# Performance work log

Hardware: AMD Instinct MI355X
Metric: run time of the kernel (lower is better)

The kernel has to match this reference:

```python
import jax, jax.numpy as jnp
import numpy as np

NUM_HEADS = 16
FOCUS_FACTOR = 1.6
HEAD_REGION = {0: 0, 1: 1, 2: 2}  # head -> region (first/middle/end)


def setup_inputs() -> dict:
    key = jax.random.key(0)
    k1, k2, k3, k4, k5 = jax.random.split(key, 5)
    B, S, D = 2, 2048, 1024
    # GPT-2 style init scale so softmax is not fully saturated
    return {
        "hidden_states": jax.random.normal(k1, (B, S, D), dtype=jnp.float32),
        "c_attn_w": jax.random.normal(k2, (D, 3 * D), dtype=jnp.float32) * 0.02,
        "c_attn_b": jax.random.normal(k3, (3 * D,), dtype=jnp.float32) * 0.02,
        "c_proj_w": jax.random.normal(k4, (D, D), dtype=jnp.float32) * 0.02,
        "c_proj_b": jax.random.normal(k5, (D,), dtype=jnp.float32) * 0.02,
    }


def _region_multipliers(seq_len: int, num_heads: int, factor: float) -> jnp.ndarray:
    """[H, S] multiplier: selected heads up-weight their token region."""
    first_end = max(1, seq_len // 3)
    second_end = max(first_end + 1, 2 * seq_len // 3)
    pos = jnp.arange(seq_len)
    regions = [
        pos < first_end,
        (pos >= first_end) & (pos < second_end),
        pos >= second_end,
    ]
    mult = np.ones((num_heads, seq_len), dtype=np.float32)
    mult = jnp.asarray(mult)
    for h, r in HEAD_REGION.items():
        if h < num_heads:
            mult = mult.at[h].set(1.0 + (factor - 1.0) * regions[r].astype(jnp.float32))
    return mult


def reference(hidden_states, c_attn_w, c_attn_b, c_proj_w, c_proj_b):
    B, S, D = hidden_states.shape
    H = NUM_HEADS
    hd = D // H

    qkv = hidden_states @ c_attn_w + c_attn_b  # [B, S, 3D]
    q, k, v = jnp.split(qkv, 3, axis=-1)

    def _reshape(x):  # [B, S, D] -> [B, H, S, hd]
        return x.reshape(B, S, H, hd).transpose(0, 2, 1, 3)

    q, k, v = _reshape(q), _reshape(k), _reshape(v)

    scores = jnp.einsum("bhqd,bhkd->bhqk", q, k) / jnp.sqrt(jnp.float32(hd))
    causal = jnp.tril(jnp.ones((S, S), dtype=bool))
    mask_value = jnp.finfo(scores.dtype).min
    scores = jnp.where(causal[None, None], scores, mask_value)

    attn = jax.nn.softmax(scores, axis=-1)  # [B, H, S, S]

    # Per-head region reweight + renorm (only for the divergent heads)
    mult = _region_multipliers(S, H, FOCUS_FACTOR)  # [H, S]
    scaled = attn * mult[None, :, None, :]
    scaled = scaled / jnp.sum(scaled, axis=-1, keepdims=True)
    div_heads = jnp.zeros((H,), dtype=bool)
    for h in HEAD_REGION:
        if h < H:
            div_heads = div_heads.at[h].set(True)
    attn = jnp.where(div_heads[None, :, None, None], scaled, attn)

    out = jnp.einsum("bhqk,bhkd->bhqd", attn, v)  # [B, H, S, hd]
    out = out.transpose(0, 2, 1, 3).reshape(B, S, D)
    out = out @ c_proj_w + c_proj_b
    return out
```

## Files before the change

kernel.cpp:

```cpp
#include <hip/hip_runtime.h>
#include <hip/hip_bf16.h>

typedef __attribute__((ext_vector_type(8))) short bf16x8;
typedef __attribute__((ext_vector_type(4))) float f32x4;
typedef __attribute__((ext_vector_type(16))) float f32x16;
typedef __attribute__((ext_vector_type(4))) unsigned int u32x4;
typedef unsigned short u16;

#define MFMA_BF16(a, b, c) __builtin_amdgcn_mfma_f32_16x16x32_bf16(a, b, c, 0, 0, 0)
#define MFMA32(a, b, c) __builtin_amdgcn_mfma_f32_32x32x16_bf16(a, b, c, 0, 0, 0)

__device__ inline u16 f2b(float x) {
  unsigned int u = __builtin_bit_cast(unsigned int, x);
  u += 0x7fffu + ((u >> 16) & 1u);
  return (u16)(u >> 16);
}

__device__ inline float exp2_fast(float x) {
  float r;
  asm("v_exp_f32 %0, %1" : "=v"(r) : "v"(x));
  return r;
}

__device__ inline unsigned int cvtpk_bf16(float lo, float hi) {
  unsigned int r;
  asm("v_cvt_pk_bf16_f32 %0, %1, %2" : "=v"(r) : "v"(lo), "v"(hi));
  return r;
}

__device__ inline void pswap(unsigned int& dst, unsigned int& src) {
  asm("v_permlane32_swap_b32 %0, %1" : "+v"(dst), "+v"(src));
}

__device__ inline void gload16(void* lds, const void* g) {
  __builtin_amdgcn_global_load_lds((const __attribute__((address_space(1))) void*)g,
                                   (__attribute__((address_space(3))) void*)lds,
                                   16, 0, 0);
}


__global__ __launch_bounds__(256) void cast_f32_bf16(const float* __restrict__ src,
                                                     u16* __restrict__ dst, int n4) {
  int i = blockIdx.x * blockDim.x + threadIdx.x;
  if (i < n4) {
    float4 v = ((const float4*)src)[i];
    ushort4 o;
    o.x = f2b(v.x); o.y = f2b(v.y); o.z = f2b(v.z); o.w = f2b(v.w);
    ((ushort4*)dst)[i] = o;
  }
}

__global__ __launch_bounds__(256) void transpose_cast(const float* __restrict__ src,
                                                      u16* __restrict__ dst, int K, int N) {
  __shared__ float t[32][33];
  int k0 = blockIdx.x * 32, n0 = blockIdx.y * 32;
  int tx = threadIdx.x, ty = threadIdx.y;
#pragma unroll
  for (int i = 0; i < 4; i++) t[ty + i * 8][tx] = src[(size_t)(k0 + ty + i * 8) * N + n0 + tx];
  __syncthreads();
#pragma unroll
  for (int i = 0; i < 4; i++)
    dst[(size_t)(n0 + ty + i * 8) * K + k0 + tx] = f2b(t[tx][ty + i * 8]);
}

#define QSCALE 0.1803368801f

__global__ __launch_bounds__(512, 2) void gemm256_qkv(
    const u16* __restrict__ A, const u16* __restrict__ BT, const float* __restrict__ bias,
    u16* __restrict__ oQ, u16* __restrict__ oK, u16* __restrict__ oVf) {
  __shared__ __align__(16) u16 As[2][256 * 64];
  __shared__ __align__(16) u16 Bs[2][256 * 64];
  const int K = 1024, NT = 16;
  int tid = threadIdx.x;
  int wv = tid >> 6, lane = tid & 63, lr = lane & 15, lg = lane >> 4;
  int wm = wv >> 2, wn = wv & 3;
  int bx = blockIdx.x % 12, by = blockIdx.x / 12;
  int m0 = by * 256, n0 = bx * 256;

  f32x4 acc[8][4] = {};

  auto stageA = [&](int buf, int kt, int h) {
#pragma unroll
    for (int g = 0; g < 2; g++) {
      int li = g * 512 + tid;
      int row = (li >> 3) + h * 128;
      int cb = ((li & 7) * 16) ^ ((row & 7) << 4);
      gload16((char*)&As[buf][0] + h * 16384 + g * 8192 + wv * 1024,
              (const char*)(A + (size_t)(m0 + row) * K + kt * 64) + cb);
    }
  };
  auto stageB = [&](int buf, int kt, int h) {
#pragma unroll
    for (int g = 0; g < 2; g++) {
      int li = g * 512 + tid;
      int row = (li >> 3) + h * 128;
      int cb = ((li & 7) * 16) ^ ((row & 7) << 4);
      gload16((char*)&Bs[buf][0] + h * 16384 + g * 8192 + wv * 1024,
              (const char*)(BT + (size_t)(n0 + row) * K + kt * 64) + cb);
    }
  };

  stageA(0, 0, 0); stageB(0, 0, 0); stageB(0, 0, 1); stageA(0, 0, 1);

  for (int t = 0; t < NT; ++t) {
    const int buf = t & 1;
    const bool last = (t == NT - 1);
    const char* Ab = (const char*)&As[buf][0];
    const char* Bb = (const char*)&Bs[buf][0];
    bf16x8 a[4][2], b0[2][2], b1[2][2];

    if (last) asm volatile("s_waitcnt vmcnt(0)" ::: "memory");
    else      asm volatile("s_waitcnt vmcnt(4)" ::: "memory");
    __builtin_amdgcn_s_barrier();
#pragma unroll
    for (int ii = 0; ii < 4; ii++) {
      int row = wm * 16 + ii * 32 + lr;
#pragma unroll
      for (int kk = 0; kk < 2; kk++)
        a[ii][kk] = *(const bf16x8*)(Ab + row * 128 + ((kk * 64 + lg * 16) ^ ((row & 7) << 4)));
    }
#pragma unroll
    for (int jj2 = 0; jj2 < 2; jj2++) {
      int row = wn * 16 + jj2 * 64 + lr;
#pragma unroll
      for (int kk = 0; kk < 2; kk++)
        b0[jj2][kk] = *(const bf16x8*)(Bb + row * 128 + ((kk * 64 + lg * 16) ^ ((row & 7) << 4)));
    }
    if (!last) stageA(buf ^ 1, t + 1, 0);
    __builtin_amdgcn_s_setprio(1);
#pragma unroll
    for (int ii = 0; ii < 4; ii++)
#pragma unroll
      for (int jj2 = 0; jj2 < 2; jj2++)
#pragma unroll
        for (int kk = 0; kk < 2; kk++)
          acc[ii][jj2] = MFMA_BF16(a[ii][kk], b0[jj2][kk], acc[ii][jj2]);
    __builtin_amdgcn_s_setprio(0);
    __builtin_amdgcn_sched_barrier(0);
    __builtin_amdgcn_s_barrier();

    if (!last) asm volatile("s_waitcnt vmcnt(4)" ::: "memory");
    __builtin_amdgcn_s_barrier();
#pragma unroll
    for (int jj2 = 0; jj2 < 2; jj2++) {
      int row = wn * 16 + jj2 * 64 + 128 + lr;
#pragma unroll
      for (int kk = 0; kk < 2; kk++)
        b1[jj2][kk] = *(const bf16x8*)(Bb + row * 128 + ((kk * 64 + lg * 16) ^ ((row & 7) << 4)));
    }
    if (!last) stageB(buf ^ 1, t + 1, 0);
    __builtin_amdgcn_s_setprio(1);
#pragma unroll
    for (int ii = 0; ii < 4; ii++)
#pragma unroll
      for (int jj2 = 0; jj2 < 2; jj2++)
#pragma unroll
        for (int kk = 0; kk < 2; kk++)
          acc[ii][2 + jj2] = MFMA_BF16(a[ii][kk], b1[jj2][kk], acc[ii][2 + jj2]);
    __builtin_amdgcn_s_setprio(0);
    __builtin_amdgcn_sched_barrier(0);
    __builtin_amdgcn_s_barrier();

    if (!last) asm volatile("s_waitcnt vmcnt(4)" ::: "memory");
    __builtin_amdgcn_s_barrier();
#pragma unroll
    for (int ii = 0; ii < 4; ii++) {
      int row = wm * 16 + ii * 32 + 128 + lr;
#pragma unroll
      for (int kk = 0; kk < 2; kk++)
        a[ii][kk] = *(const bf16x8*)(Ab + row * 128 + ((kk * 64 + lg * 16) ^ ((row & 7) << 4)));
    }
    if (!last) stageB(buf ^ 1, t + 1, 1);
    __builtin_amdgcn_s_setprio(1);
#pragma unroll
    for (int ii = 0; ii < 4; ii++)
#pragma unroll
      for (int jj2 = 0; jj2 < 2; jj2++)
#pragma unroll
        for (int kk = 0; kk < 2; kk++)
          acc[4 + ii][jj2] = MFMA_BF16(a[ii][kk], b0[jj2][kk], acc[4 + ii][jj2]);
    __builtin_amdgcn_s_setprio(0);
    __builtin_amdgcn_sched_barrier(0);
    __builtin_amdgcn_s_barrier();

    if (!last) stageA(buf ^ 1, t + 1, 1);
    __builtin_amdgcn_s_setprio(1);
#pragma unroll
    for (int ii = 0; ii < 4; ii++)
#pragma unroll
      for (int jj2 = 0; jj2 < 2; jj2++)
#pragma unroll
        for (int kk = 0; kk < 2; kk++)
          acc[4 + ii][2 + jj2] = MFMA_BF16(a[ii][kk], b1[jj2][kk], acc[4 + ii][2 + jj2]);
    __builtin_amdgcn_s_setprio(0);
    __builtin_amdgcn_sched_barrier(0);
    __builtin_amdgcn_s_barrier();
  }

#pragma unroll
  for (int i = 0; i < 8; i++) {
#pragma unroll
    for (int j = 0; j < 4; j++) {
#pragma unroll
      for (int jj = 0; jj < 4; jj++) {
        int row = m0 + wm * 16 + (i & 3) * 32 + (i >> 2) * 128 + lg * 4 + jj;
        int col = n0 + wn * 16 + (j & 1) * 64 + (j >> 1) * 128 + lr;
        float v = acc[i][j][jj] + bias[col];
        int bb = row >> 11, s = row & 2047;
        int tile = s >> 6, key = s & 63;
        if (col < 1024) {
          oQ[((size_t)((bb * 16 + (col >> 6)) * 2048 + s)) * 64 + (col & 63)] = f2b(v * QSCALE);
        } else if (col < 2048) {
          int c = col - 1024;
          int hh = c >> 6, d = c & 63;
          int jf = ((key >> 5) << 2) + (d >> 4);
          int ln = (((d >> 3) & 1) << 5) | (key & 31);
          oK[(size_t)(bb * 16 + hh) * 131072 + tile * 4096 + jf * 512 + ln * 8 + (d & 7)] =
              f2b(v);
        } else {
          int c = col - 2048;
          int hh = c >> 6, d = c & 63;
          int jf = ((d >> 5) << 2) + (key >> 4);
          int ln = (((key >> 3) & 1) << 5) | (d & 31);
          oVf[(size_t)(bb * 16 + hh) * 131072 + tile * 4096 + jf * 512 + ln * 8 + (key & 7)] =
              f2b(v);
        }
      }
    }
  }
}

__global__ __launch_bounds__(256) void gemm_bt_f32(
    const u16* __restrict__ A, const u16* __restrict__ BT, const float* __restrict__ bias,
    float* __restrict__ oF, int M, int N, int K, int nbx) {
  __shared__ __align__(16) u16 As[128 * 64];
  __shared__ __align__(16) u16 Bs[128 * 64];
  int tid = threadIdx.x;
  int wv = tid >> 6, lane = tid & 63, lr = lane & 15, lg = lane >> 4;
  int bx = blockIdx.x % nbx, by = blockIdx.x / nbx;
  int m0 = by * 128, n0 = bx * 128;
  int wr = (wv >> 1) * 64, wc = (wv & 1) * 64;

  f32x4 acc[4][4] = {};

  for (int k0 = 0; k0 < K; k0 += 64) {
#pragma unroll
    for (int j = 0; j < 4; j++) {
      int li = j * 256 + tid;
      int row = li >> 3;
      int cb = ((li & 7) * 16) ^ ((row & 7) << 4);
      gload16((char*)As + j * 4096 + wv * 1024,
              (const char*)(A + (size_t)(m0 + row) * K + k0) + cb);
      gload16((char*)Bs + j * 4096 + wv * 1024,
              (const char*)(BT + (size_t)(n0 + row) * K + k0) + cb);
    }
    __syncthreads();
#pragma unroll
    for (int kk = 0; kk < 2; kk++) {
      bf16x8 a[4], b[4];
#pragma unroll
      for (int i = 0; i < 4; i++) {
        int row = wr + i * 16 + lr;
        a[i] = *(const bf16x8*)((const char*)As + row * 128 +
                                ((kk * 64 + lg * 16) ^ ((row & 7) << 4)));
      }
#pragma unroll
      for (int j = 0; j < 4; j++) {
        int row = wc + j * 16 + lr;
        b[j] = *(const bf16x8*)((const char*)Bs + row * 128 +
                                ((kk * 64 + lg * 16) ^ ((row & 7) << 4)));
      }
#pragma unroll
      for (int i = 0; i < 4; i++)
#pragma unroll
        for (int j = 0; j < 4; j++) acc[i][j] = MFMA_BF16(a[i], b[j], acc[i][j]);
    }
    __syncthreads();
  }

#pragma unroll
  for (int i = 0; i < 4; i++)
#pragma unroll
    for (int j = 0; j < 4; j++)
#pragma unroll
      for (int jj = 0; jj < 4; jj++) {
        int row = m0 + wr + i * 16 + lg * 4 + jj;
        int col = n0 + wc + j * 16 + lr;
        oF[(size_t)row * N + col] = acc[i][j][jj] + bias[col];
      }
}

#define SEQL 2048
#define FIRST_END 682
#define SECOND_END 1365
#define LOG2F16 0.6780719051f

__global__ __launch_bounds__(256) void attn_kernel(const u16* __restrict__ Qb,
                                                   const u16* __restrict__ Kf,
                                                   const u16* __restrict__ Vf,
                                                   u16* __restrict__ AO) {
  __shared__ float Ol[4][16][66];
  __shared__ float Ml[4][32], Ll[4][32], Cl[4][32];

  int tid = threadIdx.x;
  int w = tid >> 6, l = tid & 63;
  int r31 = l & 31, hi = l >> 5;

  int xcd = blockIdx.x & 7, slot = blockIdx.x >> 3;
  int bh = xcd * 4 + (slot >> 6);
  int qt = 63 - (slot & 63);
  int q0 = qt * 32;
  int h = bh & 15, b = bh >> 4;

  const u16* Qp = Qb + ((size_t)bh * SEQL + q0 + r31) * 64 + hi * 8;
  bf16x8 qa[4];
#pragma unroll
  for (int kb = 0; kb < 4; kb++) qa[kb] = *(const bf16x8*)(Qp + kb * 16);

  const u16* Kfp = Kf + (size_t)bh * 131072;
  const u16* Vfp = Vf + (size_t)bh * 131072;

  f32x16 o0 = {}, o1 = {};
  float m = -1e30f, lsum = 0.f;

  const int N = (q0 + 95) >> 6;
  const bool hasb = (h < 3);

  for (int t = w; t < N; t += 4) {
    const int kv0 = t << 6;
    const bool last = (t == N - 1);
    const u16* kt = Kfp + (size_t)t * 4096;
    const u16* vt = Vfp + (size_t)t * 4096;

    bf16x8 ka[4], kb2[4];
#pragma unroll
    for (int kb = 0; kb < 4; kb++) {
      ka[kb]  = *(const bf16x8*)(kt + kb * 512 + l * 8);
      kb2[kb] = *(const bf16x8*)(kt + (4 + kb) * 512 + l * 8);
    }
    f32x16 sA = {}, sB = {};
#pragma unroll
    for (int kb = 0; kb < 4; kb++) sA = MFMA32(ka[kb], qa[kb], sA);
#pragma unroll
    for (int kb = 0; kb < 4; kb++) sB = MFMA32(kb2[kb], qa[kb], sB);

    if (hasb) {
#pragma unroll
      for (int r = 0; r < 16; r++) {
        int kA = kv0 + ((r & 3) + 8 * (r >> 2) + 4 * hi);
        int kB = kA + 32;
        int rA = (kA < FIRST_END) ? 0 : (kA < SECOND_END) ? 1 : 2;
        int rB = (kB < FIRST_END) ? 0 : (kB < SECOND_END) ? 1 : 2;
        if (rA == h) sA[r] += LOG2F16;
        if (rB == h) sB[r] += LOG2F16;
      }
    }
    if (last) {
      int q = q0 + r31;
#pragma unroll
      for (int r = 0; r < 16; r++) {
        int kA = kv0 + ((r & 3) + 8 * (r >> 2) + 4 * hi);
        if (kA > q) sA[r] = -1e30f;
        if (kA + 32 > q) sB[r] = -1e30f;
      }
    }

#define MAX4(v, i) fmaxf(fmaxf(v[i], v[i + 1]), fmaxf(v[i + 2], v[i + 3]))
    float mA = fmaxf(fmaxf(MAX4(sA, 0), MAX4(sA, 4)), fmaxf(MAX4(sA, 8), MAX4(sA, 12)));
    float mB = fmaxf(fmaxf(MAX4(sB, 0), MAX4(sB, 4)), fmaxf(MAX4(sB, 8), MAX4(sB, 12)));
    float mx = fmaxf(mA, mB);
    mx = fmaxf(mx, __shfl_xor(mx, 32));
    float mn = fmaxf(m, mx);
    float corr = exp2_fast(m - mn);
    m = mn;

    unsigned int wA[8], wB[8];
    float s0 = 0.f, s1 = 0.f;
#pragma unroll
    for (int i = 0; i < 8; i++) {
      float pa0 = exp2_fast(sA[2 * i] - mn), pa1 = exp2_fast(sA[2 * i + 1] - mn);
      float pb0 = exp2_fast(sB[2 * i] - mn), pb1 = exp2_fast(sB[2 * i + 1] - mn);
      s0 += pa0 + pa1;
      s1 += pb0 + pb1;
      wA[i] = cvtpk_bf16(pa0, pa1);
      wB[i] = cvtpk_bf16(pb0, pb1);
    }
    float ssum = s0 + s1;
    ssum += __shfl_xor(ssum, 32);
    lsum = lsum * corr + ssum;
    o0 *= corr;
    o1 *= corr;

    pswap(wA[0], wA[2]); pswap(wA[1], wA[3]);
    pswap(wA[4], wA[6]); pswap(wA[5], wA[7]);
    pswap(wB[0], wB[2]); pswap(wB[1], wB[3]);
    pswap(wB[4], wB[6]); pswap(wB[5], wB[7]);

    bf16x8 pb[4];
    pb[0] = __builtin_bit_cast(bf16x8, (u32x4){wA[0], wA[1], wA[2], wA[3]});
    pb[1] = __builtin_bit_cast(bf16x8, (u32x4){wA[4], wA[5], wA[6], wA[7]});
    pb[2] = __builtin_bit_cast(bf16x8, (u32x4){wB[0], wB[1], wB[2], wB[3]});
    pb[3] = __builtin_bit_cast(bf16x8, (u32x4){wB[4], wB[5], wB[6], wB[7]});

#pragma unroll
    for (int c = 0; c < 4; c++) {
      bf16x8 va0 = *(const bf16x8*)(vt + c * 512 + l * 8);
      bf16x8 va1 = *(const bf16x8*)(vt + (4 + c) * 512 + l * 8);
      o0 = MFMA32(va0, pb[c], o0);
      o1 = MFMA32(va1, pb[c], o1);
    }
  }

  Ml[w][r31] = m;
  Ll[w][r31] = lsum;
#pragma unroll
  for (int r = 0; r < 16; r++) Ol[w][r][l] = o0[r];
  __syncthreads();

  if (tid < 128) {
    int w2 = tid >> 5, q = tid & 31;
    float m0 = Ml[0][q], m1 = Ml[1][q], m2 = Ml[2][q], m3 = Ml[3][q];
    float ms = fmaxf(fmaxf(m0, m1), fmaxf(m2, m3));
    float e0 = exp2_fast(m0 - ms), e1 = exp2_fast(m1 - ms);
    float e2 = exp2_fast(m2 - ms), e3 = exp2_fast(m3 - ms);
    float ls = Ll[0][q] * e0 + Ll[1][q] * e1 + Ll[2][q] * e2 + Ll[3][q] * e3;
    float ei = (w2 == 0) ? e0 : (w2 == 1) ? e1 : (w2 == 2) ? e2 : e3;
    Cl[w2][q] = ei / ls;
  }
  __syncthreads();

  int mq = tid >> 3, md = (tid & 7) * 4;
  float c0 = Cl[0][mq], c1 = Cl[1][mq], c2 = Cl[2][mq], c3 = Cl[3][mq];
  u16* aop = AO + ((size_t)(b * SEQL + q0 + mq)) * 1024 + h * 64;

  {
    u16 ov[4];
#pragma unroll
    for (int j = 0; j < 4; j++) {
      int d = md + j;
      int h2 = (d >> 2) & 1, rr = (d & 3) + 4 * (d >> 3);
      int ll2 = mq + 32 * h2;
      ov[j] = f2b(Ol[0][rr][ll2] * c0 + Ol[1][rr][ll2] * c1 +
                  Ol[2][rr][ll2] * c2 + Ol[3][rr][ll2] * c3);
    }
    *(uint2*)(aop + md) = *(const uint2*)ov;
  }
  __syncthreads();
#pragma unroll
  for (int r = 0; r < 16; r++) Ol[w][r][l] = o1[r];
  __syncthreads();
  {
    u16 ov[4];
#pragma unroll
    for (int j = 0; j < 4; j++) {
      int d = md + j;
      int h2 = (d >> 2) & 1, rr = (d & 3) + 4 * (d >> 3);
      int ll2 = mq + 32 * h2;
      ov[j] = f2b(Ol[0][rr][ll2] * c0 + Ol[1][rr][ll2] * c1 +
                  Ol[2][rr][ll2] * c2 + Ol[3][rr][ll2] * c3);
    }
    *(uint2*)(aop + 32 + md) = *(const uint2*)ov;
  }
}


extern "C" void kernel_launch(void* const* d_in, const int* in_sizes, int n_in,
                              void* d_out, int out_size, void* d_ws, size_t ws_size,
                              hipStream_t stream) {
  const float* hs = (const float*)d_in[0];
  const float* w1 = (const float*)d_in[1];
  const float* b1 = (const float*)d_in[2];
  const float* w2 = (const float*)d_in[3];
  const float* b2 = (const float*)d_in[4];
  float* out = (float*)d_out;

  char* ws = (char*)d_ws;
  const size_t MB = 1u << 20;
  u16* hsb = (u16*)(ws + 0);
  u16* w1t = (u16*)(ws + 8 * MB);
  u16* w2t = (u16*)(ws + 14 * MB);
  u16* Qb = (u16*)(ws + 16 * MB);
  u16* Kf = (u16*)(ws + 24 * MB);
  u16* Vf = (u16*)(ws + 32 * MB);
  u16* AO = hsb;

  cast_f32_bf16<<<4096, 256, 0, stream>>>(hs, hsb, 4096 * 1024 / 4);
  dim3 tb(32, 8);
  transpose_cast<<<dim3(32, 96), tb, 0, stream>>>(w1, w1t, 1024, 3072);
  transpose_cast<<<dim3(32, 32), tb, 0, stream>>>(w2, w2t, 1024, 1024);

  gemm256_qkv<<<16 * 12, 512, 0, stream>>>(hsb, w1t, b1, Qb, Kf, Vf);
  attn_kernel<<<2048, 256, 0, stream>>>(Qb, Kf, Vf, AO);
  gemm_bt_f32<<<32 * 8, 256, 0, stream>>>(AO, w2t, b2, out, 4096, 1024, 1024, 8);
}
```

Baseline: 131.9 us.

## Double-buffer output projection GEMM and merge QKV GEMM phases into two halves

The output projection GEMM moves from a single-buffered loop with two __syncthreads per k-step to a double-buffered LDS pipeline. Global loads for the next k-tile are issued while MFMAs run on the current one, and launch bounds now allow two blocks per CU. In the QKV GEMM, four barrier-separated compute phases per k-tile become two, each loading more operands and issuing larger MFMA batches. The aim is to cut barrier and wait overhead and hide global latency, at the cost of more LDS, more live registers, and a retuned vmcnt wait scheme.

```diff
diff --git a/kernel.cpp b/kernel.cpp
--- a/kernel.cpp
+++ b/kernel.cpp
@@ -109,89 +109,65 @@
     const char* Bb = (const char*)&Bs[buf][0];
     bf16x8 a[4][2], b0[2][2], b1[2][2];
 
+    asm volatile("s_waitcnt vmcnt(2)" ::: "memory");
+    __builtin_amdgcn_s_barrier();
+#pragma unroll
+    for (int ii = 0; ii < 4; ii++) {
+      int row = wm * 16 + ii * 32 + lr;
+#pragma unroll
+      for (int kk = 0; kk < 2; kk++)
+        a[ii][kk] = *(const bf16x8*)(Ab + row * 128 + ((kk * 64 + lg * 16) ^ ((row & 7) << 4)));
+    }
+#pragma unroll
+    for (int jj2 = 0; jj2 < 2; jj2++) {
+      int row = wn * 16 + jj2 * 64 + lr;
+#pragma unroll
+      for (int kk = 0; kk < 2; kk++)
+        b0[jj2][kk] = *(const bf16x8*)(Bb + row * 128 + ((kk * 64 + lg * 16) ^ ((row & 7) << 4)));
+    }
+#pragma unroll
+    for (int jj2 = 0; jj2 < 2; jj2++) {
+      int row = wn * 16 + jj2 * 64 + 128 + lr;
+#pragma unroll
+      for (int kk = 0; kk < 2; kk++)
+        b1[jj2][kk] = *(const bf16x8*)(Bb + row * 128 + ((kk * 64 + lg * 16) ^ ((row & 7) << 4)));
+    }
+    if (!last) { stageA(buf ^ 1, t + 1, 0); stageB(buf ^ 1, t + 1, 0); }
+    __builtin_amdgcn_s_setprio(1);
+#pragma unroll
+    for (int ii = 0; ii < 4; ii++)
+#pragma unroll
+      for (int jj2 = 0; jj2 < 2; jj2++)
+#pragma unroll
+        for (int kk = 0; kk < 2; kk++) {
+          acc[ii][jj2] = MFMA_BF16(a[ii][kk], b0[jj2][kk], acc[ii][jj2]);
+          acc[ii][2 + jj2] = MFMA_BF16(a[ii][kk], b1[jj2][kk], acc[ii][2 + jj2]);
+        }
+    __builtin_amdgcn_s_setprio(0);
+    __builtin_amdgcn_sched_barrier(0);
+    __builtin_amdgcn_s_barrier();
+
     if (last) asm volatile("s_waitcnt vmcnt(0)" ::: "memory");
     else      asm volatile("s_waitcnt vmcnt(4)" ::: "memory");
     __builtin_amdgcn_s_barrier();
 #pragma unroll
     for (int ii = 0; ii < 4; ii++) {
-      int row = wm * 16 + ii * 32 + lr;
+      int row = wm * 16 + ii * 32 + 128 + lr;
 #pragma unroll
       for (int kk = 0; kk < 2; kk++)
         a[ii][kk] = *(const bf16x8*)(Ab + row * 128 + ((kk * 64 + lg * 16) ^ ((row & 7) << 4)));
     }
-#pragma unroll
-    for (int jj2 = 0; jj2 < 2; jj2++) {
-      int row = wn * 16 + jj2 * 64 + lr;
-#pragma unroll
-      for (int kk = 0; kk < 2; kk++)
-        b0[jj2][kk] = *(const bf16x8*)(Bb + row * 128 + ((kk * 64 + lg * 16) ^ ((row & 7) << 4)));
-    }
-    if (!last) stageA(buf ^ 1, t + 1, 0);
+    if (!last) { stageB(buf ^ 1, t + 1, 1); stageA(buf ^ 1, t + 1, 1); }
     __builtin_amdgcn_s_setprio(1);
 #pragma unroll
     for (int ii = 0; ii < 4; ii++)
 #pragma unroll
       for (int jj2 = 0; jj2 < 2; jj2++)
 #pragma unroll
-        for (int kk = 0; kk < 2; kk++)
-          acc[ii][jj2] = MFMA_BF16(a[ii][kk], b0[jj2][kk], acc[ii][jj2]);
-    __builtin_amdgcn_s_setprio(0);
-    __builtin_amdgcn_sched_barrier(0);
-    __builtin_amdgcn_s_barrier();
-
-    if (!last) asm volatile("s_waitcnt vmcnt(4)" ::: "memory");
-    __builtin_amdgcn_s_barrier();
-#pragma unroll
-    for (int jj2 = 0; jj2 < 2; jj2++) {
-      int row = wn * 16 + jj2 * 64 + 128 + lr;
-#pragma unroll
-      for (int kk = 0; kk < 2; kk++)
-        b1[jj2][kk] = *(const bf16x8*)(Bb + row * 128 + ((kk * 64 + lg * 16) ^ ((row & 7) << 4)));
-    }
-    if (!last) stageB(buf ^ 1, t + 1, 0);
-    __builtin_amdgcn_s_setprio(1);
-#pragma unroll
-    for (int ii = 0; ii < 4; ii++)
-#pragma unroll
-      for (int jj2 = 0; jj2 < 2; jj2++)
-#pragma unroll
-        for (int kk = 0; kk < 2; kk++)
-          acc[ii][2 + jj2] = MFMA_BF16(a[ii][kk], b1[jj2][kk], acc[ii][2 + jj2]);
-    __builtin_amdgcn_s_setprio(0);
-    __builtin_amdgcn_sched_barrier(0);
-    __builtin_amdgcn_s_barrier();
-
-    if (!last) asm volatile("s_waitcnt vmcnt(4)" ::: "memory");
-    __builtin_amdgcn_s_barrier();
-#pragma unroll
-    for (int ii = 0; ii < 4; ii++) {
-      int row = wm * 16 + ii * 32 + 128 + lr;
-#pragma unroll
-      for (int kk = 0; kk < 2; kk++)
-        a[ii][kk] = *(const bf16x8*)(Ab + row * 128 + ((kk * 64 + lg * 16) ^ ((row & 7) << 4)));
-    }
-    if (!last) stageB(buf ^ 1, t + 1, 1);
-    __builtin_amdgcn_s_setprio(1);
-#pragma unroll
-    for (int ii = 0; ii < 4; ii++)
-#pragma unroll
-      for (int jj2 = 0; jj2 < 2; jj2++)
-#pragma unroll
-        for (int kk = 0; kk < 2; kk++)
+        for (int kk = 0; kk < 2; kk++) {
           acc[4 + ii][jj2] = MFMA_BF16(a[ii][kk], b0[jj2][kk], acc[4 + ii][jj2]);
-    __builtin_amdgcn_s_setprio(0);
-    __builtin_amdgcn_sched_barrier(0);
-    __builtin_amdgcn_s_barrier();
-
-    if (!last) stageA(buf ^ 1, t + 1, 1);
-    __builtin_amdgcn_s_setprio(1);
-#pragma unroll
-    for (int ii = 0; ii < 4; ii++)
-#pragma unroll
-      for (int jj2 = 0; jj2 < 2; jj2++)
-#pragma unroll
-        for (int kk = 0; kk < 2; kk++)
           acc[4 + ii][2 + jj2] = MFMA_BF16(a[ii][kk], b1[jj2][kk], acc[4 + ii][2 + jj2]);
+        }
     __builtin_amdgcn_s_setprio(0);
     __builtin_amdgcn_sched_barrier(0);
     __builtin_amdgcn_s_barrier();
@@ -230,52 +206,112 @@
   }
 }
 
-__global__ __launch_bounds__(256) void gemm_bt_f32(
+__global__ __launch_bounds__(256, 2) void gemm_bt_f32(
     const u16* __restrict__ A, const u16* __restrict__ BT, const float* __restrict__ bias,
     float* __restrict__ oF, int M, int N, int K, int nbx) {
-  __shared__ __align__(16) u16 As[128 * 64];
-  __shared__ __align__(16) u16 Bs[128 * 64];
+  __shared__ __align__(16) u16 As[2][128 * 64];
+  __shared__ __align__(16) u16 Bs[2][128 * 64];
+  const int NT = 16;
   int tid = threadIdx.x;
   int wv = tid >> 6, lane = tid & 63, lr = lane & 15, lg = lane >> 4;
+  int wm = wv >> 1, wn = wv & 1;
   int bx = blockIdx.x % nbx, by = blockIdx.x / nbx;
   int m0 = by * 128, n0 = bx * 128;
-  int wr = (wv >> 1) * 64, wc = (wv & 1) * 64;
 
   f32x4 acc[4][4] = {};
 
-  for (int k0 = 0; k0 < K; k0 += 64) {
-#pragma unroll
-    for (int j = 0; j < 4; j++) {
-      int li = j * 256 + tid;
-      int row = li >> 3;
+  auto stageA = [&](int buf, int kt, int h) {
+#pragma unroll
+    for (int g = 0; g < 2; g++) {
+      int li = g * 256 + tid;
+      int row = (li >> 3) + h * 64;
       int cb = ((li & 7) * 16) ^ ((row & 7) << 4);
-      gload16((char*)As + j * 4096 + wv * 1024,
-              (const char*)(A + (size_t)(m0 + row) * K + k0) + cb);
-      gload16((char*)Bs + j * 4096 + wv * 1024,
-              (const char*)(BT + (size_t)(n0 + row) * K + k0) + cb);
-    }
-    __syncthreads();
-#pragma unroll
-    for (int kk = 0; kk < 2; kk++) {
-      bf16x8 a[4], b[4];
-#pragma unroll
-      for (int i = 0; i < 4; i++) {
-        int row = wr + i * 16 + lr;
-        a[i] = *(const bf16x8*)((const char*)As + row * 128 +
-                                ((kk * 64 + lg * 16) ^ ((row & 7) << 4)));
-      }
-#pragma unroll
-      for (int j = 0; j < 4; j++) {
-        int row = wc + j * 16 + lr;
-        b[j] = *(const bf16x8*)((const char*)Bs + row * 128 +
-                                ((kk * 64 + lg * 16) ^ ((row & 7) << 4)));
-      }
-#pragma unroll
-      for (int i = 0; i < 4; i++)
-#pragma unroll
-        for (int j = 0; j < 4; j++) acc[i][j] = MFMA_BF16(a[i], b[j], acc[i][j]);
-    }
-    __syncthreads();
+      gload16((char*)&As[buf][0] + h * 8192 + g * 4096 + wv * 1024,
+              (const char*)(A + (size_t)(m0 + row) * K + kt * 64) + cb);
+    }
+  };
+  auto stageB = [&](int buf, int kt, int h) {
+#pragma unroll
+    for (int g = 0; g < 2; g++) {
+      int li = g * 256 + tid;
+      int row = (li >> 3) + h * 64;
+      int cb = ((li & 7) * 16) ^ ((row & 7) << 4);
+      gload16((char*)&Bs[buf][0] + h * 8192 + g * 4096 + wv * 1024,
+              (const char*)(BT + (size_t)(n0 + row) * K + kt * 64) + cb);
+    }
+  };
+
+  stageA(0, 0, 0); stageB(0, 0, 0); stageB(0, 0, 1); stageA(0, 0, 1);
+
+  for (int t = 0; t < NT; ++t) {
+    const int buf = t & 1;
+    const bool last = (t == NT - 1);
+    const char* Ab = (const char*)&As[buf][0];
+    const char* Bb = (const char*)&Bs[buf][0];
+    bf16x8 a[2][2], b0[2][2], b1[2][2];
+
+    asm volatile("s_waitcnt vmcnt(2)" ::: "memory");
+    __builtin_amdgcn_s_barrier();
+#pragma unroll
+    for (int ii = 0; ii < 2; ii++) {
+      int row = wm * 16 + ii * 32 + lr;
+#pragma unroll
+      for (int kk = 0; kk < 2; kk++)
+        a[ii][kk] = *(const bf16x8*)(Ab + row * 128 + ((kk * 64 + lg * 16) ^ ((row & 7) << 4)));
+    }
+#pragma unroll
+    for (int jj2 = 0; jj2 < 2; jj2++) {
+      int row = wn * 16 + jj2 * 32 + lr;
+#pragma unroll
+      for (int kk = 0; kk < 2; kk++)
+        b0[jj2][kk] = *(const bf16x8*)(Bb + row * 128 + ((kk * 64 + lg * 16) ^ ((row & 7) << 4)));
+    }
+#pragma unroll
+    for (int jj2 = 0; jj2 < 2; jj2++) {
+      int row = wn * 16 + jj2 * 32 + 64 + lr;
+#pragma unroll
+      for (int kk = 0; kk < 2; kk++)
+        b1[jj2][kk] = *(const bf16x8*)(Bb + row * 128 + ((kk * 64 + lg * 16) ^ ((row & 7) << 4)));
+    }
+    if (!last) { stageA(buf ^ 1, t + 1, 0); stageB(buf ^ 1, t + 1, 0); }
+    __builtin_amdgcn_s_setprio(1);
+#pragma unroll
+    for (int ii = 0; ii < 2; ii++)
+#pragma unroll
+      for (int jj2 = 0; jj2 < 2; jj2++)
+#pragma unroll
+        for (int kk = 0; kk < 2; kk++) {
+          acc[ii][jj2] = MFMA_BF16(a[ii][kk], b0[jj2][kk], acc[ii][jj2]);
+          acc[ii][2 + jj2] = MFMA_BF16(a[ii][kk], b1[jj2][kk], acc[ii][2 + jj2]);
+        }
+    __builtin_amdgcn_s_setprio(0);
+    __builtin_amdgcn_sched_barrier(0);
+    __builtin_amdgcn_s_barrier();
+
+    if (last) asm volatile("s_waitcnt vmcnt(0)" ::: "memory");
+    else      asm volatile("s_waitcnt vmcnt(4)" ::: "memory");
+    __builtin_amdgcn_s_barrier();
+#pragma unroll
+    for (int ii = 0; ii < 2; ii++) {
+      int row = wm * 16 + ii * 32 + 64 + lr;
+#pragma unroll
+      for (int kk = 0; kk < 2; kk++)
+        a[ii][kk] = *(const bf16x8*)(Ab + row * 128 + ((kk * 64 + lg * 16) ^ ((row & 7) << 4)));
+    }
+    if (!last) { stageB(buf ^ 1, t + 1, 1); stageA(buf ^ 1, t + 1, 1); }
+    __builtin_amdgcn_s_setprio(1);
+#pragma unroll
+    for (int ii = 0; ii < 2; ii++)
+#pragma unroll
+      for (int jj2 = 0; jj2 < 2; jj2++)
+#pragma unroll
+        for (int kk = 0; kk < 2; kk++) {
+          acc[2 + ii][jj2] = MFMA_BF16(a[ii][kk], b0[jj2][kk], acc[2 + ii][jj2]);
+          acc[2 + ii][2 + jj2] = MFMA_BF16(a[ii][kk], b1[jj2][kk], acc[2 + ii][2 + jj2]);
+        }
+    __builtin_amdgcn_s_setprio(0);
+    __builtin_amdgcn_sched_barrier(0);
+    __builtin_amdgcn_s_barrier();
   }
 
 #pragma unroll
@@ -284,8 +320,8 @@
     for (int j = 0; j < 4; j++)
 #pragma unroll
       for (int jj = 0; jj < 4; jj++) {
-        int row = m0 + wr + i * 16 + lg * 4 + jj;
-        int col = n0 + wc + j * 16 + lr;
+        int row = m0 + wm * 16 + (i & 1) * 32 + (i >> 1) * 64 + lg * 4 + jj;
+        int col = n0 + wn * 16 + (j & 1) * 32 + (j >> 1) * 64 + lr;
         oF[(size_t)row * N + col] = acc[i][j][jj] + bias[col];
       }
 }
```

New measurement: 123.6 us. 1.07x faster.
